# Kernel optimization log

Measured on AMD Instinct MI355X. Metric: run time of the kernel, lower is better.

The kernel has to match this reference:

```python
import jax, jax.numpy as jnp
import numpy as np

N_NODES = 50000
N_EDGES = 800000
IN_CH, HID_CH, OUT_CH = 128, 256, 128


def _glorot(key, shape):
    fan_in, fan_out = shape[1], shape[0]
    lim = float(np.sqrt(6.0 / (fan_in + fan_out)))
    return jax.random.uniform(key, shape, jnp.float32, -lim, lim)


def setup_inputs() -> dict:
    key = jax.random.key(0)
    ks = jax.random.split(key, 8)
    x = jax.random.normal(ks[0], (N_NODES, IN_CH), jnp.float32)
    edge_index = jax.random.randint(ks[1], (2, N_EDGES), 0, N_NODES, jnp.int64)
    return {
        "x": x,
        "edge_index": edge_index,
        # layer 1: SAGEConv(128 -> 256): lin_l (with bias) on aggregated, lin_r (no bias) on root
        "W1l": _glorot(ks[2], (HID_CH, IN_CH)),
        "b1l": jnp.zeros((HID_CH,), jnp.float32),
        "W1r": _glorot(ks[3], (HID_CH, IN_CH)),
        # layer 2: SAGEConv(256 -> 128)
        "W2l": _glorot(ks[4], (OUT_CH, HID_CH)),
        "b2l": jnp.zeros((OUT_CH,), jnp.float32),
        "W2r": _glorot(ks[5], (OUT_CH, HID_CH)),
    }


def _sage_conv(x, src, dst, Wl, bl, Wr, n_nodes):
    # mean-aggregate neighbor (source) features at destination nodes
    msg = x[src]                                                   # [E, C] gather
    agg = jax.ops.segment_sum(msg, dst, num_segments=n_nodes)      # [N, C]
    deg = jax.ops.segment_sum(jnp.ones((src.shape[0],), x.dtype), dst,
                              num_segments=n_nodes)                # [N]
    mean = agg / jnp.maximum(deg, 1.0)[:, None]                    # zero-degree -> 0
    return mean @ Wl.T + bl + x @ Wr.T


def reference(x, edge_index, W1l, b1l, W1r, W2l, b2l, W2r):
    src, dst = edge_index[0], edge_index[1]
    n = x.shape[0]
    h = _sage_conv(x, src, dst, W1l, b1l, W1r, n)
    h = jax.nn.relu(h)  # dropout is identity in eval mode
    out = _sage_conv(h, src, dst, W2l, b2l, W2r, n)
    return out
```

## Files before the change

### kernel.cpp

```cpp
#include <hip/hip_runtime.h>

#define N_NODES 50000
#define IN_CH   128
#define HID_CH  256
#define OUT_CH  128

#define NB    196
#define NWG   256
#define NBNW  (NB * NWG)

#define XBLK  3125
#define WBLK  64

typedef __attribute__((ext_vector_type(8))) short bf16x8;
typedef __attribute__((ext_vector_type(4))) float f32x4;
typedef __attribute__((ext_vector_type(2))) float f32x2;

__device__ __forceinline__ unsigned short f32_bf16_rne(float f) {
    unsigned u = __float_as_uint(f);
    unsigned r = u + 0x7fff + ((u >> 16) & 1);
    return (unsigned short)(r >> 16);
}

__device__ __forceinline__ void cvt8(const float* __restrict__ in,
                                     unsigned short* __restrict__ outp, size_t j)
{
    const float4* p = reinterpret_cast<const float4*>(in) + 2 * j;
    float4 a = p[0], b = p[1];
    alignas(16) unsigned short t[8] = {
        f32_bf16_rne(a.x), f32_bf16_rne(a.y), f32_bf16_rne(a.z), f32_bf16_rne(a.w),
        f32_bf16_rne(b.x), f32_bf16_rne(b.y), f32_bf16_rne(b.z), f32_bf16_rne(b.w)};
    *reinterpret_cast<int4*>(outp + 8 * j) = *reinterpret_cast<const int4*>(t);
}

__global__ __launch_bounds__(256) void prep_kernel(
    const int* __restrict__ src, const int* __restrict__ dst,
    int* __restrict__ counts, int E, int chunk,
    const float* __restrict__ x, unsigned short* __restrict__ xb,
    unsigned char* __restrict__ xb8,
    const float* __restrict__ W1l, const float* __restrict__ W1r,
    const float* __restrict__ W2l, const float* __restrict__ W2r,
    unsigned short* __restrict__ W1lb, unsigned short* __restrict__ W1rb,
    unsigned short* __restrict__ W2lb, unsigned short* __restrict__ W2rb)
{
    const int b = blockIdx.x;
    if (b < NWG) {
        __shared__ int h[NB];
        for (int i = threadIdx.x; i < NB; i += 256) h[i] = 0;
        __syncthreads();
        const int e0 = b * chunk;
        const int e1 = min(e0 + chunk, E);
        for (int e = e0 + threadIdx.x; e < e1; e += 256) {
            int s = src[e], d = dst[e];
            if ((unsigned)s < (unsigned)N_NODES && (unsigned)d < (unsigned)N_NODES)
                atomicAdd(&h[d >> 8], 1);
        }
        __syncthreads();
        for (int i = threadIdx.x; i < NB; i += 256)
            counts[i * NWG + b] = h[i];
    } else if (b < NWG + XBLK) {
        size_t j = (size_t)(b - NWG) * 256 + threadIdx.x;
        const float4* p = reinterpret_cast<const float4*>(x) + 2 * j;
        float4 a = p[0], bb = p[1];
        alignas(16) unsigned short t[8] = {
            f32_bf16_rne(a.x),  f32_bf16_rne(a.y),  f32_bf16_rne(a.z),  f32_bf16_rne(a.w),
            f32_bf16_rne(bb.x), f32_bf16_rne(bb.y), f32_bf16_rne(bb.z), f32_bf16_rne(bb.w)};
        *reinterpret_cast<int4*>(xb + 8 * j) = *reinterpret_cast<const int4*>(t);
        unsigned u0 = __builtin_amdgcn_cvt_pk_fp8_f32(a.x, a.y, 0, false);
        u0 = __builtin_amdgcn_cvt_pk_fp8_f32(a.z, a.w, u0, true);
        unsigned u1 = __builtin_amdgcn_cvt_pk_fp8_f32(bb.x, bb.y, 0, false);
        u1 = __builtin_amdgcn_cvt_pk_fp8_f32(bb.z, bb.w, u1, true);
        uint2 uv; uv.x = u0; uv.y = u1;
        *reinterpret_cast<uint2*>(xb8 + 8 * j) = uv;
    } else {
        int idx = (b - NWG - XBLK) * 256 + threadIdx.x;
        int seg = idx >> 12, j = idx & 4095;
        const float* in = (seg == 0) ? W1l : (seg == 1) ? W1r : (seg == 2) ? W2l : W2r;
        unsigned short* o = (seg == 0) ? W1lb : (seg == 1) ? W1rb : (seg == 2) ? W2lb : W2rb;
        cvt8(in, o, (size_t)j);
    }
}

__global__ __launch_bounds__(256) void scan_kernel(
    const int* __restrict__ counts, int* __restrict__ S)
{
    __shared__ int red[256];
    const int t = threadIdx.x;
    const int b = blockIdx.x;
    const int lim = b * NWG;
    int partial = 0;
    for (int i = t; i < lim; i += 256) partial += counts[i];
    red[t] = partial;
    __syncthreads();
    for (int off = 128; off >= 1; off >>= 1) {
        if (t < off) red[t] += red[t + off];
        __syncthreads();
    }
    const int base_b = red[0];
    __syncthreads();
    const int v = counts[b * NWG + t];
    red[t] = v;
    __syncthreads();
    for (int off = 1; off < 256; off <<= 1) {
        int u = (t >= off) ? red[t - off] : 0;
        __syncthreads();
        if (t >= off) red[t] += u;
        __syncthreads();
    }
    S[b * NWG + t] = base_b + red[t] - v;
    if (b == NB - 1 && t == 255) S[NBNW] = base_b + red[255];
}

__global__ __launch_bounds__(256) void bscatter_kernel(
    const int* __restrict__ src, const int* __restrict__ dst,
    const int* __restrict__ S, int* __restrict__ pairs, int E, int chunk)
{
    __shared__ int cur[NB];
    const int w = blockIdx.x;
    for (int i = threadIdx.x; i < NB; i += 256) cur[i] = S[i * NWG + w];
    __syncthreads();
    const int e0 = w * chunk;
    const int e1 = min(e0 + chunk, E);
    for (int e = e0 + threadIdx.x; e < e1; e += 256) {
        int s = src[e], d = dst[e];
        if ((unsigned)s < (unsigned)N_NODES && (unsigned)d < (unsigned)N_NODES) {
            int pos = atomicAdd(&cur[d >> 8], 1);
            pairs[pos] = (s << 8) | (d & 255);
        }
    }
}

__global__ __launch_bounds__(256) void bsort_kernel(
    const int* __restrict__ pairs, const int* __restrict__ S,
    int* __restrict__ rowptr, int* __restrict__ colidx)
{
    __shared__ int hcnt[256];
    __shared__ int hcur[256];
    const int b = blockIdx.x;
    const int start = S[b * NWG];
    const int endv  = (b == NB - 1) ? S[NBNW] : S[(b + 1) * NWG];

    hcnt[threadIdx.x] = 0;
    __syncthreads();
    for (int e = start + threadIdx.x; e < endv; e += 256)
        atomicAdd(&hcnt[pairs[e] & 255], 1);
    __syncthreads();
    for (int off = 1; off < 256; off <<= 1) {
        int t = (threadIdx.x >= off) ? hcnt[threadIdx.x - off] : 0;
        __syncthreads();
        if (threadIdx.x >= off) hcnt[threadIdx.x] += t;
        __syncthreads();
    }
    int offv = (threadIdx.x == 0) ? 0 : hcnt[threadIdx.x - 1];
    hcur[threadIdx.x] = offv;
    int node = (b << 8) + threadIdx.x;
    if (node < N_NODES) rowptr[node] = start + offv;
    if (b == NB - 1 && threadIdx.x == 0) rowptr[N_NODES] = endv;
    __syncthreads();
    for (int e = start + threadIdx.x; e < endv; e += 256) {
        int p = pairs[e];
        int pos = atomicAdd(&hcur[p & 255], 1);
        colidx[start + pos] = (unsigned)p >> 8;
    }
}

#define ACC8(v)                                                              \
    { f32x2 t0 = __builtin_amdgcn_cvt_pk_f32_fp8(v.x, false);                \
      f32x2 t1 = __builtin_amdgcn_cvt_pk_f32_fp8(v.x, true);                 \
      f32x2 t2 = __builtin_amdgcn_cvt_pk_f32_fp8(v.y, false);                \
      f32x2 t3 = __builtin_amdgcn_cvt_pk_f32_fp8(v.y, true);                 \
      acc[0] += t0.x; acc[1] += t0.y; acc[2] += t1.x; acc[3] += t1.y;        \
      acc[4] += t2.x; acc[5] += t2.y; acc[6] += t3.x; acc[7] += t3.y; }

#define LDROW(s, CH) (*reinterpret_cast<const uint2*>(feat + (size_t)(s) * (CH) + l8 * 8))

#define AGG_BODY(CH)                                                            \
    const int node = blockIdx.x * 16 + (threadIdx.x >> 4);                      \
    if (node >= N_NODES) return;                                                \
    const int l8 = threadIdx.x & 15;                                            \
    const int beg = rowptr[node], end = rowptr[node + 1];                       \
    const int len = end - beg;                                                  \
    float acc[8] = {};                                                          \
    for (int base = beg; base < end; base += 16) {                              \
        const int cnt = min(16, end - base);                                    \
        int ci = colidx[base + ((l8 < cnt) ? l8 : 0)];                          \
        int k = 0;                                                              \
        for (; k + 7 < cnt; k += 8) {                                           \
            int s0 = __shfl(ci, k, 16),     s1 = __shfl(ci, k + 1, 16);         \
            int s2 = __shfl(ci, k + 2, 16), s3 = __shfl(ci, k + 3, 16);         \
            int s4 = __shfl(ci, k + 4, 16), s5 = __shfl(ci, k + 5, 16);         \
            int s6 = __shfl(ci, k + 6, 16), s7 = __shfl(ci, k + 7, 16);         \
            uint2 v0 = LDROW(s0, CH); uint2 v1 = LDROW(s1, CH);                 \
            uint2 v2 = LDROW(s2, CH); uint2 v3 = LDROW(s3, CH);                 \
            uint2 v4 = LDROW(s4, CH); uint2 v5 = LDROW(s5, CH);                 \
            uint2 v6 = LDROW(s6, CH); uint2 v7 = LDROW(s7, CH);                 \
            ACC8(v0) ACC8(v1) ACC8(v2) ACC8(v3)                                 \
            ACC8(v4) ACC8(v5) ACC8(v6) ACC8(v7)                                 \
        }                                                                       \
        for (; k + 3 < cnt; k += 4) {                                           \
            int s0 = __shfl(ci, k, 16),     s1 = __shfl(ci, k + 1, 16);         \
            int s2 = __shfl(ci, k + 2, 16), s3 = __shfl(ci, k + 3, 16);         \
            uint2 v0 = LDROW(s0, CH); uint2 v1 = LDROW(s1, CH);                 \
            uint2 v2 = LDROW(s2, CH); uint2 v3 = LDROW(s3, CH);                 \
            ACC8(v0) ACC8(v1) ACC8(v2) ACC8(v3)                                 \
        }                                                                       \
        for (; k < cnt; ++k) {                                                  \
            int s0 = __shfl(ci, k, 16);                                         \
            uint2 v0 = LDROW(s0, CH);                                           \
            ACC8(v0)                                                            \
        }                                                                       \
    }                                                                           \
    const float sc = 1.0f / fmaxf((float)len, 1.0f);

__global__ __launch_bounds__(256) void agg1_kernel(
    const unsigned char* __restrict__ feat, const int* __restrict__ rowptr,
    const int* __restrict__ colidx, unsigned short* __restrict__ outp)
{
    AGG_BODY(IN_CH)
    alignas(16) unsigned short t[8];
#pragma unroll
    for (int k = 0; k < 8; ++k) t[k] = f32_bf16_rne(acc[k] * sc);
    *reinterpret_cast<int4*>(outp + (size_t)node * IN_CH + l8 * 8) =
        *reinterpret_cast<const int4*>(t);
}

__global__ __launch_bounds__(256) void agg2_kernel(
    const unsigned char* __restrict__ feat, const int* __restrict__ rowptr,
    const int* __restrict__ colidx, const unsigned short* __restrict__ hrb,
    const float* __restrict__ b2l, float* __restrict__ out)
{
    AGG_BODY(OUT_CH)
    const int4 hv = *reinterpret_cast<const int4*>(hrb + (size_t)node * OUT_CH + l8 * 8);
    const unsigned short* hs = reinterpret_cast<const unsigned short*>(&hv);
    float4 b0 = *reinterpret_cast<const float4*>(b2l + l8 * 8);
    float4 b1 = *reinterpret_cast<const float4*>(b2l + l8 * 8 + 4);
    float4 o0, o1;
    o0.x = acc[0] * sc + __uint_as_float((unsigned)hs[0] << 16) + b0.x;
    o0.y = acc[1] * sc + __uint_as_float((unsigned)hs[1] << 16) + b0.y;
    o0.z = acc[2] * sc + __uint_as_float((unsigned)hs[2] << 16) + b0.z;
    o0.w = acc[3] * sc + __uint_as_float((unsigned)hs[3] << 16) + b0.w;
    o1.x = acc[4] * sc + __uint_as_float((unsigned)hs[4] << 16) + b1.x;
    o1.y = acc[5] * sc + __uint_as_float((unsigned)hs[5] << 16) + b1.y;
    o1.z = acc[6] * sc + __uint_as_float((unsigned)hs[6] << 16) + b1.z;
    o1.w = acc[7] * sc + __uint_as_float((unsigned)hs[7] << 16) + b1.w;
    float* o = out + (size_t)node * OUT_CH + l8 * 8;
    reinterpret_cast<float4*>(o)[0] = o0;
    reinterpret_cast<float4*>(o)[1] = o1;
}

__device__ __forceinline__ void stage_async(
    const unsigned short* __restrict__ g, int ldg, int rowBase, int maxRow,
    int kBase, unsigned short* __restrict__ s, int tid)
{
    const int wave = tid >> 6;
    const int lane = tid & 63;
    const int r_in = lane >> 3;
    const int c_g  = (lane & 7) ^ r_in;
#pragma unroll
    for (int it = 0; it < 4; ++it) {
        const int rowBlk = it * 32 + wave * 8;
        int row = rowBase + rowBlk + r_in;
        if (row >= maxRow) row = maxRow - 1;
        const unsigned short* gp = g + (size_t)row * ldg + kBase + c_g * 8;
        unsigned short* lp = s + rowBlk * 64;
        __builtin_amdgcn_global_load_lds(
            (const __attribute__((address_space(1))) unsigned int*)gp,
            (__attribute__((address_space(3))) unsigned int*)lp,
            16, 0, 0);
    }
}

__device__ __forceinline__ const bf16x8* frag_ptr(
    const unsigned short* __restrict__ s, int rr, int c)
{
    return reinterpret_cast<const bf16x8*>(s + rr * 64 + (((c ^ (rr & 7))) << 3));
}

__device__ __forceinline__ void mfma_tile(
    const unsigned short* __restrict__ As, const unsigned short* __restrict__ Bs,
    int wm, int wn, int l16, int quad, f32x4 acc[4][4])
{
#pragma unroll
    for (int k0 = 0; k0 < 64; k0 += 32) {
        const int c = (k0 >> 3) + quad;
        bf16x8 a[4], b[4];
#pragma unroll
        for (int i = 0; i < 4; ++i)
            a[i] = *frag_ptr(As, wm * 64 + i * 16 + l16, c);
#pragma unroll
        for (int j = 0; j < 4; ++j)
            b[j] = *frag_ptr(Bs, wn * 64 + j * 16 + l16, c);
#pragma unroll
        for (int i = 0; i < 4; ++i)
#pragma unroll
            for (int j = 0; j < 4; ++j)
                acc[i][j] = __builtin_amdgcn_mfma_f32_16x16x32_bf16(
                    b[j], a[i], acc[i][j], 0, 0, 0);
    }
}

__global__ __launch_bounds__(256) void gemm1_mfma(
    const unsigned short* __restrict__ mean1b, const unsigned short* __restrict__ xb,
    const unsigned short* __restrict__ W1lb,   const unsigned short* __restrict__ W1rb,
    const float* __restrict__ b1l, unsigned short* __restrict__ hb)
{
    __shared__ unsigned short As[128 * 64];
    __shared__ unsigned short Bs[128 * 64];
    const int tid = threadIdx.x;
    const int wid = tid >> 6, lane = tid & 63;
    const int wm = wid & 1, wn = wid >> 1;
    const int l16 = lane & 15, quad = lane >> 4;
    const int rowBase = blockIdx.x * 128;
    const int colBase = blockIdx.y * 128;

    f32x4 z = {0.f, 0.f, 0.f, 0.f};
    f32x4 acc[4][4];
#pragma unroll
    for (int i = 0; i < 4; ++i)
#pragma unroll
        for (int j = 0; j < 4; ++j) acc[i][j] = z;

#pragma unroll
    for (int op = 0; op < 2; ++op) {
        const unsigned short* A = op ? xb : mean1b;
        const unsigned short* B = op ? W1rb : W1lb;
#pragma unroll
        for (int kb = 0; kb < IN_CH; kb += 64) {
            __syncthreads();
            stage_async(A, IN_CH, rowBase, N_NODES, kb, As, tid);
            stage_async(B, IN_CH, colBase, HID_CH, kb, Bs, tid);
            __syncthreads();
            mfma_tile(As, Bs, wm, wn, l16, quad, acc);
        }
    }

#pragma unroll
    for (int i = 0; i < 4; ++i) {
        int m = rowBase + wm * 64 + i * 16 + l16;
        if (m >= N_NODES) continue;
#pragma unroll
        for (int j = 0; j < 4; ++j) {
            int col = colBase + wn * 64 + j * 16 + quad * 4;
            float4 bv = *reinterpret_cast<const float4*>(b1l + col);
            alignas(8) unsigned short t[4];
            t[0] = f32_bf16_rne(fmaxf(acc[i][j][0] + bv.x, 0.0f));
            t[1] = f32_bf16_rne(fmaxf(acc[i][j][1] + bv.y, 0.0f));
            t[2] = f32_bf16_rne(fmaxf(acc[i][j][2] + bv.z, 0.0f));
            t[3] = f32_bf16_rne(fmaxf(acc[i][j][3] + bv.w, 0.0f));
            *reinterpret_cast<uint2*>(hb + (size_t)m * HID_CH + col) =
                *reinterpret_cast<const uint2*>(t);
        }
    }
}

__global__ __launch_bounds__(256) void gemm2_mfma(
    const unsigned short* __restrict__ hb, const unsigned short* __restrict__ W2lb,
    const unsigned short* __restrict__ W2rb,
    unsigned char* __restrict__ pb8, unsigned short* __restrict__ hrb)
{
    __shared__ unsigned short As[128 * 64];
    __shared__ unsigned short Bs[128 * 64];
    const int tid = threadIdx.x;
    const int wid = tid >> 6, lane = tid & 63;
    const int wm = wid & 1, wn = wid >> 1;
    const int l16 = lane & 15, quad = lane >> 4;
    const int rowBase = blockIdx.x * 128;
    const unsigned short* B = blockIdx.y ? W2rb : W2lb;

    f32x4 z = {0.f, 0.f, 0.f, 0.f};
    f32x4 acc[4][4];
#pragma unroll
    for (int i = 0; i < 4; ++i)
#pragma unroll
        for (int j = 0; j < 4; ++j) acc[i][j] = z;

#pragma unroll
    for (int kb = 0; kb < HID_CH; kb += 64) {
        __syncthreads();
        stage_async(hb, HID_CH, rowBase, N_NODES, kb, As, tid);
        stage_async(B, HID_CH, 0, OUT_CH, kb, Bs, tid);
        __syncthreads();
        mfma_tile(As, Bs, wm, wn, l16, quad, acc);
    }

    if (blockIdx.y == 0) {
#pragma unroll
        for (int i = 0; i < 4; ++i) {
            int m = rowBase + wm * 64 + i * 16 + l16;
            if (m >= N_NODES) continue;
#pragma unroll
            for (int j = 0; j < 4; ++j) {
                int col = wn * 64 + j * 16 + quad * 4;
                unsigned u = __builtin_amdgcn_cvt_pk_fp8_f32(
                    acc[i][j][0], acc[i][j][1], 0, false);
                u = __builtin_amdgcn_cvt_pk_fp8_f32(
                    acc[i][j][2], acc[i][j][3], u, true);
                *reinterpret_cast<unsigned*>(pb8 + (size_t)m * OUT_CH + col) = u;
            }
        }
    } else {
#pragma unroll
        for (int i = 0; i < 4; ++i) {
            int m = rowBase + wm * 64 + i * 16 + l16;
            if (m >= N_NODES) continue;
#pragma unroll
            for (int j = 0; j < 4; ++j) {
                int col = wn * 64 + j * 16 + quad * 4;
                alignas(8) unsigned short t[4];
                t[0] = f32_bf16_rne(acc[i][j][0]);
                t[1] = f32_bf16_rne(acc[i][j][1]);
                t[2] = f32_bf16_rne(acc[i][j][2]);
                t[3] = f32_bf16_rne(acc[i][j][3]);
                *reinterpret_cast<uint2*>(hrb + (size_t)m * OUT_CH + col) =
                    *reinterpret_cast<const uint2*>(t);
            }
        }
    }
}

extern "C" void kernel_launch(void* const* d_in, const int* in_sizes, int n_in,
                              void* d_out, int out_size, void* d_ws, size_t ws_size,
                              hipStream_t stream)
{
    const float* x   = (const float*)d_in[0];
    const int*   ei  = (const int*)d_in[1];
    const float* W1l = (const float*)d_in[2];
    const float* b1l = (const float*)d_in[3];
    const float* W1r = (const float*)d_in[4];
    const float* W2l = (const float*)d_in[5];
    const float* b2l = (const float*)d_in[6];
    const float* W2r = (const float*)d_in[7];

    const int E = in_sizes[1] / 2;
    const int* src = ei;
    const int* dst = ei + E;

    char* ws = (char*)d_ws;
    size_t off = 0;
    auto alloc = [&](size_t bytes) {
        void* p = ws + off;
        off += (bytes + 255) & ~(size_t)255;
        return p;
    };
    unsigned short* xb     = (unsigned short*)alloc((size_t)N_NODES * IN_CH * 2);
    unsigned char*  xb8    = (unsigned char*)alloc((size_t)N_NODES * IN_CH);
    unsigned short* mean1b = (unsigned short*)alloc((size_t)N_NODES * IN_CH * 2);
    unsigned short* hb     = (unsigned short*)alloc((size_t)N_NODES * HID_CH * 2);
    unsigned char*  pb8    = (unsigned char*)alloc((size_t)N_NODES * OUT_CH);
    unsigned short* hrb    = (unsigned short*)alloc((size_t)N_NODES * OUT_CH * 2);
    unsigned short* W1lb   = (unsigned short*)alloc((size_t)HID_CH * IN_CH * 2);
    unsigned short* W1rb   = (unsigned short*)alloc((size_t)HID_CH * IN_CH * 2);
    unsigned short* W2lb   = (unsigned short*)alloc((size_t)OUT_CH * HID_CH * 2);
    unsigned short* W2rb   = (unsigned short*)alloc((size_t)OUT_CH * HID_CH * 2);
    int* counts = (int*)alloc((size_t)NBNW * 4);
    int* S      = (int*)alloc((size_t)(NBNW + 1) * 4);
    int* pairs  = (int*)alloc((size_t)E * 4);
    int* rowptr = (int*)alloc((size_t)(N_NODES + 1) * 4);
    int* colidx = (int*)alloc((size_t)E * 4);
    float* out = (float*)d_out;

    const int chunk = (E + NWG - 1) / NWG;

    prep_kernel<<<NWG + XBLK + WBLK, 256, 0, stream>>>(
        src, dst, counts, E, chunk, x, xb, xb8,
        W1l, W1r, W2l, W2r, W1lb, W1rb, W2lb, W2rb);
    scan_kernel<<<NB, 256, 0, stream>>>(counts, S);
    bscatter_kernel<<<NWG, 256, 0, stream>>>(src, dst, S, pairs, E, chunk);
    bsort_kernel<<<NB, 256, 0, stream>>>(pairs, S, rowptr, colidx);

    const int aggBlocks = (N_NODES + 15) / 16;
    const int mBlocks = (N_NODES + 127) / 128;

    agg1_kernel<<<aggBlocks, 256, 0, stream>>>(xb8, rowptr, colidx, mean1b);
    gemm1_mfma<<<dim3(mBlocks, HID_CH / 128), 256, 0, stream>>>(
        mean1b, xb, W1lb, W1rb, b1l, hb);
    gemm2_mfma<<<dim3(mBlocks, 2), 256, 0, stream>>>(hb, W2lb, W2rb, pb8, hrb);
    agg2_kernel<<<aggBlocks, 256, 0, stream>>>(pb8, rowptr, colidx, hrb, b2l, out);
}
```

Baseline: 223.7 us.

## Concatenate GEMM operands along K and widen blocks to full output width

Layer-1 now uses one interleaved [mean | x] A buffer (K=256) and a concatenated [W1l | W1r] B matrix, so gemm1 runs a single K loop. Each 512-thread block covers all 256 output columns, which means the A tile is loaded once instead of once per column block. Gemm2 similarly stacks W2l and W2r into one 256-row B matrix, so a single block writes both outputs and hb is read once. This lowers redundant A-tile traffic and launch grid size, at the cost of larger shared memory, bigger blocks and fewer blocks in flight.

```diff
diff --git a/kernel.cpp b/kernel.cpp
--- a/kernel.cpp
+++ b/kernel.cpp
@@ -22,26 +22,25 @@
     return (unsigned short)(r >> 16);
 }
 
-__device__ __forceinline__ void cvt8(const float* __restrict__ in,
-                                     unsigned short* __restrict__ outp, size_t j)
-{
-    const float4* p = reinterpret_cast<const float4*>(in) + 2 * j;
+__device__ __forceinline__ void cvt8_io(const float* __restrict__ inp,
+                                        unsigned short* __restrict__ outp)
+{
+    const float4* p = reinterpret_cast<const float4*>(inp);
     float4 a = p[0], b = p[1];
     alignas(16) unsigned short t[8] = {
         f32_bf16_rne(a.x), f32_bf16_rne(a.y), f32_bf16_rne(a.z), f32_bf16_rne(a.w),
         f32_bf16_rne(b.x), f32_bf16_rne(b.y), f32_bf16_rne(b.z), f32_bf16_rne(b.w)};
-    *reinterpret_cast<int4*>(outp + 8 * j) = *reinterpret_cast<const int4*>(t);
+    *reinterpret_cast<int4*>(outp) = *reinterpret_cast<const int4*>(t);
 }
 
 __global__ __launch_bounds__(256) void prep_kernel(
     const int* __restrict__ src, const int* __restrict__ dst,
     int* __restrict__ counts, int E, int chunk,
-    const float* __restrict__ x, unsigned short* __restrict__ xb,
+    const float* __restrict__ x, unsigned short* __restrict__ A1,
     unsigned char* __restrict__ xb8,
     const float* __restrict__ W1l, const float* __restrict__ W1r,
     const float* __restrict__ W2l, const float* __restrict__ W2r,
-    unsigned short* __restrict__ W1lb, unsigned short* __restrict__ W1rb,
-    unsigned short* __restrict__ W2lb, unsigned short* __restrict__ W2rb)
+    unsigned short* __restrict__ B1, unsigned short* __restrict__ W2cat)
 {
     const int b = blockIdx.x;
     if (b < NWG) {
@@ -65,7 +64,9 @@
         alignas(16) unsigned short t[8] = {
             f32_bf16_rne(a.x),  f32_bf16_rne(a.y),  f32_bf16_rne(a.z),  f32_bf16_rne(a.w),
             f32_bf16_rne(bb.x), f32_bf16_rne(bb.y), f32_bf16_rne(bb.z), f32_bf16_rne(bb.w)};
-        *reinterpret_cast<int4*>(xb + 8 * j) = *reinterpret_cast<const int4*>(t);
+        const size_t node = j >> 4, chunk16 = j & 15;
+        *reinterpret_cast<int4*>(A1 + node * 256 + 128 + chunk16 * 8) =
+            *reinterpret_cast<const int4*>(t);
         unsigned u0 = __builtin_amdgcn_cvt_pk_fp8_f32(a.x, a.y, 0, false);
         u0 = __builtin_amdgcn_cvt_pk_fp8_f32(a.z, a.w, u0, true);
         unsigned u1 = __builtin_amdgcn_cvt_pk_fp8_f32(bb.x, bb.y, 0, false);
@@ -75,9 +76,19 @@
     } else {
         int idx = (b - NWG - XBLK) * 256 + threadIdx.x;
         int seg = idx >> 12, j = idx & 4095;
-        const float* in = (seg == 0) ? W1l : (seg == 1) ? W1r : (seg == 2) ? W2l : W2r;
-        unsigned short* o = (seg == 0) ? W1lb : (seg == 1) ? W1rb : (seg == 2) ? W2lb : W2rb;
-        cvt8(in, o, (size_t)j);
+        if (seg == 0) {
+            int row = j >> 4, cb = (j & 15) * 8;
+            cvt8_io(W1l + (size_t)j * 8, B1 + (size_t)row * 256 + cb);
+        } else if (seg == 1) {
+            int row = j >> 4, cb = (j & 15) * 8;
+            cvt8_io(W1r + (size_t)j * 8, B1 + (size_t)row * 256 + 128 + cb);
+        } else if (seg == 2) {
+            int row = j >> 5, cb = (j & 31) * 8;
+            cvt8_io(W2l + (size_t)j * 8, W2cat + (size_t)row * 256 + cb);
+        } else {
+            int row = j >> 5, cb = (j & 31) * 8;
+            cvt8_io(W2r + (size_t)j * 8, W2cat + (size_t)(128 + row) * 256 + cb);
+        }
     }
 }
 
@@ -214,13 +225,13 @@
 
 __global__ __launch_bounds__(256) void agg1_kernel(
     const unsigned char* __restrict__ feat, const int* __restrict__ rowptr,
-    const int* __restrict__ colidx, unsigned short* __restrict__ outp)
+    const int* __restrict__ colidx, unsigned short* __restrict__ A1)
 {
     AGG_BODY(IN_CH)
     alignas(16) unsigned short t[8];
 #pragma unroll
     for (int k = 0; k < 8; ++k) t[k] = f32_bf16_rne(acc[k] * sc);
-    *reinterpret_cast<int4*>(outp + (size_t)node * IN_CH + l8 * 8) =
+    *reinterpret_cast<int4*>(A1 + (size_t)node * 256 + l8 * 8) =
         *reinterpret_cast<const int4*>(t);
 }
 
@@ -248,7 +259,8 @@
     reinterpret_cast<float4*>(o)[1] = o1;
 }
 
-__device__ __forceinline__ void stage_async(
+template <int NIT>
+__device__ __forceinline__ void stage8(
     const unsigned short* __restrict__ g, int ldg, int rowBase, int maxRow,
     int kBase, unsigned short* __restrict__ s, int tid)
 {
@@ -257,8 +269,8 @@
     const int r_in = lane >> 3;
     const int c_g  = (lane & 7) ^ r_in;
 #pragma unroll
-    for (int it = 0; it < 4; ++it) {
-        const int rowBlk = it * 32 + wave * 8;
+    for (int it = 0; it < NIT; ++it) {
+        const int rowBlk = it * 64 + wave * 8;
         int row = rowBase + rowBlk + r_in;
         if (row >= maxRow) row = maxRow - 1;
         const unsigned short* gp = g + (size_t)row * ldg + kBase + c_g * 8;
@@ -299,19 +311,17 @@
     }
 }
 
-__global__ __launch_bounds__(256) void gemm1_mfma(
-    const unsigned short* __restrict__ mean1b, const unsigned short* __restrict__ xb,
-    const unsigned short* __restrict__ W1lb,   const unsigned short* __restrict__ W1rb,
+__global__ __launch_bounds__(512) void gemm1_mfma(
+    const unsigned short* __restrict__ A1, const unsigned short* __restrict__ B1,
     const float* __restrict__ b1l, unsigned short* __restrict__ hb)
 {
     __shared__ unsigned short As[128 * 64];
-    __shared__ unsigned short Bs[128 * 64];
+    __shared__ unsigned short Bs[256 * 64];
     const int tid = threadIdx.x;
     const int wid = tid >> 6, lane = tid & 63;
     const int wm = wid & 1, wn = wid >> 1;
     const int l16 = lane & 15, quad = lane >> 4;
     const int rowBase = blockIdx.x * 128;
-    const int colBase = blockIdx.y * 128;
 
     f32x4 z = {0.f, 0.f, 0.f, 0.f};
     f32x4 acc[4][4];
@@ -321,17 +331,12 @@
         for (int j = 0; j < 4; ++j) acc[i][j] = z;
 
 #pragma unroll
-    for (int op = 0; op < 2; ++op) {
-        const unsigned short* A = op ? xb : mean1b;
-        const unsigned short* B = op ? W1rb : W1lb;
-#pragma unroll
-        for (int kb = 0; kb < IN_CH; kb += 64) {
-            __syncthreads();
-            stage_async(A, IN_CH, rowBase, N_NODES, kb, As, tid);
-            stage_async(B, IN_CH, colBase, HID_CH, kb, Bs, tid);
-            __syncthreads();
-            mfma_tile(As, Bs, wm, wn, l16, quad, acc);
-        }
+    for (int kb = 0; kb < 256; kb += 64) {
+        __syncthreads();
+        stage8<2>(A1, 256, rowBase, N_NODES, kb, As, tid);
+        stage8<4>(B1, 256, 0, HID_CH, kb, Bs, tid);
+        __syncthreads();
+        mfma_tile(As, Bs, wm, wn, l16, quad, acc);
     }
 
 #pragma unroll
@@ -340,7 +345,7 @@
         if (m >= N_NODES) continue;
 #pragma unroll
         for (int j = 0; j < 4; ++j) {
-            int col = colBase + wn * 64 + j * 16 + quad * 4;
+            int col = wn * 64 + j * 16 + quad * 4;
             float4 bv = *reinterpret_cast<const float4*>(b1l + col);
             alignas(8) unsigned short t[4];
             t[0] = f32_bf16_rne(fmaxf(acc[i][j][0] + bv.x, 0.0f));
@@ -353,19 +358,17 @@
     }
 }
 
-__global__ __launch_bounds__(256) void gemm2_mfma(
-    const unsigned short* __restrict__ hb, const unsigned short* __restrict__ W2lb,
-    const unsigned short* __restrict__ W2rb,
+__global__ __launch_bounds__(512) void gemm2_mfma(
+    const unsigned short* __restrict__ hb, const unsigned short* __restrict__ W2cat,
     unsigned char* __restrict__ pb8, unsigned short* __restrict__ hrb)
 {
     __shared__ unsigned short As[128 * 64];
-    __shared__ unsigned short Bs[128 * 64];
+    __shared__ unsigned short Bs[256 * 64];
     const int tid = threadIdx.x;
     const int wid = tid >> 6, lane = tid & 63;
     const int wm = wid & 1, wn = wid >> 1;
     const int l16 = lane & 15, quad = lane >> 4;
     const int rowBase = blockIdx.x * 128;
-    const unsigned short* B = blockIdx.y ? W2rb : W2lb;
 
     f32x4 z = {0.f, 0.f, 0.f, 0.f};
     f32x4 acc[4][4];
@@ -377,13 +380,13 @@
 #pragma unroll
     for (int kb = 0; kb < HID_CH; kb += 64) {
         __syncthreads();
-        stage_async(hb, HID_CH, rowBase, N_NODES, kb, As, tid);
-        stage_async(B, HID_CH, 0, OUT_CH, kb, Bs, tid);
+        stage8<2>(hb, HID_CH, rowBase, N_NODES, kb, As, tid);
+        stage8<4>(W2cat, HID_CH, 0, 256, kb, Bs, tid);
         __syncthreads();
         mfma_tile(As, Bs, wm, wn, l16, quad, acc);
     }
 
-    if (blockIdx.y == 0) {
+    if (wn < 2) {
 #pragma unroll
         for (int i = 0; i < 4; ++i) {
             int m = rowBase + wm * 64 + i * 16 + l16;
@@ -405,7 +408,7 @@
             if (m >= N_NODES) continue;
 #pragma unroll
             for (int j = 0; j < 4; ++j) {
-                int col = wn * 64 + j * 16 + quad * 4;
+                int col = wn * 64 + j * 16 + quad * 4 - 128;
                 alignas(8) unsigned short t[4];
                 t[0] = f32_bf16_rne(acc[i][j][0]);
                 t[1] = f32_bf16_rne(acc[i][j][1]);
@@ -442,16 +445,13 @@
         off += (bytes + 255) & ~(size_t)255;
         return p;
     };
-    unsigned short* xb     = (unsigned short*)alloc((size_t)N_NODES * IN_CH * 2);
+    unsigned short* A1     = (unsigned short*)alloc((size_t)N_NODES * 256 * 2);
     unsigned char*  xb8    = (unsigned char*)alloc((size_t)N_NODES * IN_CH);
-    unsigned short* mean1b = (unsigned short*)alloc((size_t)N_NODES * IN_CH * 2);
     unsigned short* hb     = (unsigned short*)alloc((size_t)N_NODES * HID_CH * 2);
     unsigned char*  pb8    = (unsigned char*)alloc((size_t)N_NODES * OUT_CH);
     unsigned short* hrb    = (unsigned short*)alloc((size_t)N_NODES * OUT_CH * 2);
-    unsigned short* W1lb   = (unsigned short*)alloc((size_t)HID_CH * IN_CH * 2);
-    unsigned short* W1rb   = (unsigned short*)alloc((size_t)HID_CH * IN_CH * 2);
-    unsigned short* W2lb   = (unsigned short*)alloc((size_t)OUT_CH * HID_CH * 2);
-    unsigned short* W2rb   = (unsigned short*)alloc((size_t)OUT_CH * HID_CH * 2);
+    unsigned short* B1     = (unsigned short*)alloc((size_t)HID_CH * 256 * 2);
+    unsigned short* W2cat  = (unsigned short*)alloc((size_t)256 * HID_CH * 2);
     int* counts = (int*)alloc((size_t)NBNW * 4);
     int* S      = (int*)alloc((size_t)(NBNW + 1) * 4);
     int* pairs  = (int*)alloc((size_t)E * 4);
@@ -462,8 +462,8 @@
     const int chunk = (E + NWG - 1) / NWG;
 
     prep_kernel<<<NWG + XBLK + WBLK, 256, 0, stream>>>(
-        src, dst, counts, E, chunk, x, xb, xb8,
-        W1l, W1r, W2l, W2r, W1lb, W1rb, W2lb, W2rb);
+        src, dst, counts, E, chunk, x, A1, xb8,
+        W1l, W1r, W2l, W2r, B1, W2cat);
     scan_kernel<<<NB, 256, 0, stream>>>(counts, S);
     bscatter_kernel<<<NWG, 256, 0, stream>>>(src, dst, S, pairs, E, chunk);
     bsort_kernel<<<NB, 256, 0, stream>>>(pairs, S, rowptr, colidx);
@@ -471,9 +471,8 @@
     const int aggBlocks = (N_NODES + 15) / 16;
     const int mBlocks = (N_NODES + 127) / 128;
 
-    agg1_kernel<<<aggBlocks, 256, 0, stream>>>(xb8, rowptr, colidx, mean1b);
-    gemm1_mfma<<<dim3(mBlocks, HID_CH / 128), 256, 0, stream>>>(
-        mean1b, xb, W1lb, W1rb, b1l, hb);
-    gemm2_mfma<<<dim3(mBlocks, 2), 256, 0, stream>>>(hb, W2lb, W2rb, pb8, hrb);
+    agg1_kernel<<<aggBlocks, 256, 0, stream>>>(xb8, rowptr, colidx, A1);
+    gemm1_mfma<<<mBlocks, 512, 0, stream>>>(A1, B1, b1l, hb);
+    gemm2_mfma<<<mBlocks, 512, 0, stream>>>(hb, W2cat, pb8, hrb);
     agg2_kernel<<<aggBlocks, 256, 0, stream>>>(pb8, rowptr, colidx, hrb, b2l, out);
 }
```

After: 213.9 us. 1.05x faster.
